# Kernel tuning notes

Measured on AMD Instinct MI355X. Metric: run time of the kernel, lower is better.

Reference implementation:

```python
import jax, jax.numpy as jnp
import numpy as np
from jax import lax

B, C, H, W = 2, 128, 192, 192
HEADS, WS, SS = 4, 8, 4
HID = 256  # int(C * expansion=2.0)
EPS = 1e-6


def _rpe_index(ws):
    coords = np.stack(np.meshgrid(np.arange(ws), np.arange(ws), indexing='ij')).reshape(2, -1)
    rel = (coords[:, :, None] - coords[:, None, :]).transpose(1, 2, 0)
    rel[:, :, 0] += ws - 1
    rel[:, :, 1] += ws - 1
    rel[:, :, 0] *= 2 * ws - 1
    return rel.sum(-1)  # (ws^2, ws^2) int index into rpe_table

RPE_IDX = _rpe_index(WS)


def _attn_mask(hp, wp, ws, ss):
    # Swin-style shifted-window mask, built once for static (hp, wp).
    img = np.zeros((hp, wp))
    cnt = 0
    for hs in (slice(0, -ws), slice(-ws, -ss), slice(-ss, None)):
        for wsl in (slice(0, -ws), slice(-ws, -ss), slice(-ss, None)):
            img[hs, wsl] = cnt
            cnt += 1
    mw = img.reshape(hp // ws, ws, wp // ws, ws).transpose(0, 2, 1, 3).reshape(-1, ws * ws)
    am = mw[:, None, :] - mw[:, :, None]
    return np.where(am != 0, -np.inf, 0.0).astype(np.float32)

MASK = jnp.asarray(_attn_mask(H, W, WS, SS))  # (nW, T, T)


def rmsnorm(x, s, b):
    # RMSNorm2d: variance over channel dim, computed in fp32.
    var = jnp.mean(jnp.square(x.astype(jnp.float32)), axis=1, keepdims=True)
    rms = jnp.sqrt(var + EPS).astype(x.dtype)
    return s[None, :, None, None] * x / rms + b[None, :, None, None]


def conv1x1(x, w, b):
    return jnp.einsum('oc,bchw->bohw', w, x) + b[None, :, None, None]


def dwconv3x3(x, w, b):
    y = lax.conv_general_dilated(x, w, (1, 1), 'SAME', feature_group_count=w.shape[0],
                                 dimension_numbers=('NCHW', 'OIHW', 'NCHW'))
    return y + b[None, :, None, None]


def gelu(x):
    return jax.nn.gelu(x, approximate=False)  # matches torch nn.GELU default (erf)


def conv_gated_block(x, s, b, w1, b1, wd, bd, w2, b2, beta):
    y = rmsnorm(x, s, b)
    y = conv1x1(y, w1, b1)
    y = dwconv3x3(y, wd, bd)
    u, v = jnp.split(y, 2, axis=1)
    y = conv1x1(u * gelu(v), w2, b2)
    return x + beta * y


def gated_ffn(x, s, b, w1, b1, w2, b2, gamma):
    y = rmsnorm(x, s, b)
    y = conv1x1(y, w1, b1)
    u, v = jnp.split(y, 2, axis=1)
    y = conv1x1(u * gelu(v), w2, b2)
    return x + gamma * y


def window_attention(x, qkv_w, qkv_b, rpe_table, proj_w, proj_b):
    b, c, h, w = x.shape
    hd = c // HEADS
    ws, ws2 = WS, WS * WS
    # H, W chosen divisible by ws, so _pad_to_window is a no-op here.
    x = jnp.roll(x, (-SS, -SS), axis=(2, 3))
    qkv = jnp.einsum('oc,bchw->bhwo', qkv_w, x) + qkv_b  # (B,H,W,3C)
    qkv = qkv.reshape(b, h // ws, ws, w // ws, ws, 3 * c).transpose(0, 1, 3, 2, 4, 5)
    qkv = qkv.reshape(-1, ws2, 3, HEADS, hd).transpose(2, 0, 3, 1, 4)  # (3, B*nW, nh, T, hd)
    q, k, v = qkv[0], qkv[1], qkv[2]
    attn = jnp.einsum('wnqd,wnkd->wnqk', q, k) * (hd ** -0.5)
    rpe = rpe_table[RPE_IDX.reshape(-1)].reshape(ws2, ws2, HEADS).transpose(2, 0, 1)  # (nh,T,T)
    nW = (h // ws) * (w // ws)
    attn = attn.reshape(b, nW, HEADS, ws2, ws2) + rpe[None, None] + MASK[None, :, None]
    attn = jax.nn.softmax(attn, axis=-1).reshape(-1, HEADS, ws2, ws2)
    out = jnp.einsum('wnqk,wnkd->wnqd', attn, v)
    out = out.transpose(0, 2, 1, 3).reshape(-1, ws2, c)
    out = out @ proj_w.T + proj_b  # nn.Linear
    out = out.reshape(b, h // ws, w // ws, ws, ws, c).transpose(0, 1, 3, 2, 4, 5).reshape(b, h, w, c)
    out = jnp.roll(out, (SS, SS), axis=(1, 2))
    return out.transpose(0, 3, 1, 2)


def setup_inputs():
    key = jax.random.key(0)
    ks = jax.random.split(key, 10)
    f = jnp.float32

    def nrm(k, shape, std=0.02):
        return jax.random.normal(k, shape, dtype=f) * std

    return {
        'x': jax.random.normal(ks[0], (B, C, H, W), dtype=f),
        'cg_s': jnp.ones((C,), f), 'cg_b': jnp.zeros((C,), f),
        'pw1_w': nrm(ks[1], (2 * HID, C)), 'pw1_b': jnp.zeros((2 * HID,), f),
        'dw_w': nrm(ks[2], (2 * HID, 1, 3, 3)), 'dw_b': jnp.zeros((2 * HID,), f),
        'pw2_w': nrm(ks[3], (C, HID)), 'pw2_b': jnp.zeros((C,), f),
        'beta': jnp.float32(0.5),
        'at_s': jnp.ones((C,), f), 'at_b': jnp.zeros((C,), f),
        'qkv_w': nrm(ks[4], (3 * C, C)), 'qkv_b': jnp.zeros((3 * C,), f),
        'rpe_table': nrm(ks[5], ((2 * WS - 1) ** 2, HEADS)),
        'proj_w': nrm(ks[6], (C, C)), 'proj_b': jnp.zeros((C,), f),
        'alpha': jnp.float32(0.5),
        'ff_s': jnp.ones((C,), f), 'ff_b': jnp.zeros((C,), f),
        'fc1_w': nrm(ks[7], (2 * HID, C)), 'fc1_b': jnp.zeros((2 * HID,), f),
        'fc2_w': nrm(ks[8], (C, HID)), 'fc2_b': jnp.zeros((C,), f),
        'gamma': jnp.float32(0.5),
    }


def reference(x, cg_s, cg_b, pw1_w, pw1_b, dw_w, dw_b, pw2_w, pw2_b, beta,
              at_s, at_b, qkv_w, qkv_b, rpe_table, proj_w, proj_b, alpha,
              ff_s, ff_b, fc1_w, fc1_b, fc2_w, fc2_b, gamma):
    x = conv_gated_block(x, cg_s, cg_b, pw1_w, pw1_b, dw_w, dw_b, pw2_w, pw2_b, beta)
    x = x + alpha * window_attention(rmsnorm(x, at_s, at_b), qkv_w, qkv_b, rpe_table, proj_w, proj_b)
    x = gated_ffn(x, ff_s, ff_b, fc1_w, fc1_b, fc2_w, fc2_b, gamma)
    return x
```

## Files before the change

kernel.cpp:

```cpp
#include <hip/hip_runtime.h>
#include <hip/hip_bf16.h>
#include <math.h>

#define HW   36864
#define BHW  73728

typedef float f32x4 __attribute__((ext_vector_type(4)));
typedef short short8 __attribute__((ext_vector_type(8)));
typedef short s16x4 __attribute__((ext_vector_type(4)));

__device__ __forceinline__ unsigned f2bf(float f) {
    unsigned u = __float_as_uint(f);
    return (u + 0x7fffu + ((u >> 16) & 1u)) >> 16;
}
__device__ __forceinline__ float bf2f(unsigned short s) {
    return __uint_as_float(((unsigned)s) << 16);
}
__device__ __forceinline__ float gelu_fast(float x) {
    float y = 1.5957691216057308f * fmaf(0.044715f * x * x, x, x);
    return x / (1.0f + __expf(-y));
}

__global__ __launch_bounds__(256)
void wconv_kernel(const float* __restrict__ w1, const float* __restrict__ w2,
                  const float* __restrict__ wq, const float* __restrict__ wp,
                  const float* __restrict__ wf1, const float* __restrict__ wf2,
                  const float* __restrict__ dww, const float* __restrict__ fb1,
                  ushort* __restrict__ o1, ushort* __restrict__ o2, ushort* __restrict__ oq,
                  ushort* __restrict__ op, ushort* __restrict__ of1, ushort* __restrict__ of2,
                  float* __restrict__ dwt, float* __restrict__ bg)
{
    int i = blockIdx.x * 256 + threadIdx.x;
    if      (i <  65536) o1 [i         ] = (ushort)f2bf(w1 [i         ]);
    else if (i <  98304) o2 [i -  65536] = (ushort)f2bf(w2 [i -  65536]);
    else if (i < 147456) oq [i -  98304] = (ushort)f2bf(wq [i -  98304]);
    else if (i < 163840) op [i - 147456] = (ushort)f2bf(wp [i - 147456]);
    else if (i < 229376) {
        int j = i - 163840;
        int col = j >> 7, k = j & 127;
        of1[j] = (ushort)f2bf(wf1[((size_t)((col & 1) * 256 + (col >> 1))) * 128 + k]);
    }
    else if (i < 262144) of2[i - 229376] = (ushort)f2bf(wf2[i - 229376]);
    else if (i < 266752) {
        int j = i - 262144;
        int tap = j >> 9, c = j & 511;
        dwt[j] = dww[c * 9 + tap];
    }
    else if (i < 267264) {
        int j = i - 266752;
        bg[j] = fb1[(j & 1) * 256 + (j >> 1)];
    }
}

__global__ __launch_bounds__(256)
void rmsnorm_t_kernel(const float* __restrict__ src, const float* __restrict__ s,
                      const float* __restrict__ bi, __hip_bfloat16* __restrict__ dst)
{
    int P = blockIdx.x * 256 + threadIdx.x;
    int b = P / HW, pp = P - b * HW;
    const float* xb = src + (size_t)b * 128 * HW + pp;
    float ss = 0.f;
#pragma unroll 8
    for (int c = 0; c < 128; ++c) { float v = xb[(size_t)c * HW]; ss = fmaf(v, v, ss); }
    float inv = 1.0f / sqrtf(ss * 0.0078125f + 1e-6f);
    unsigned* drow = (unsigned*)(dst + (size_t)P * 128);
#pragma unroll 4
    for (int c = 0; c < 128; c += 2) {
        float v0 = fmaf(s[c]     * xb[(size_t)c * HW],       inv, bi[c]);
        float v1 = fmaf(s[c + 1] * xb[(size_t)(c + 1) * HW], inv, bi[c + 1]);
        drow[c >> 1] = f2bf(v0) | (f2bf(v1) << 16);
    }
}

template<int K, int MODE>
__global__ __launch_bounds__(256)
void gemm_kernel(const __hip_bfloat16* __restrict__ Abf, const __hip_bfloat16* __restrict__ Wbf,
                 const float* __restrict__ bias, int N,
                 __hip_bfloat16* __restrict__ outb)
{
    __shared__ char smem[12288];
    short* sA = (short*)smem;
    short* sB = sA + 2048;

    const short* A = (const short*)Abf;
    const short* W = (const short*)Wbf;

    int t = threadIdx.x;
    int lane = t & 63, wv = t >> 6;
    int m0 = blockIdx.x * 64;
    int n0 = blockIdx.y * 128;
    int q = lane >> 4, r16 = lane & 15;

    f32x4 acc[4][2];
#pragma unroll
    for (int nt = 0; nt < 2; ++nt) {
        float bv = bias[n0 + wv * 32 + nt * 16 + r16];
#pragma unroll
        for (int mt = 0; mt < 4; ++mt) acc[mt][nt] = (f32x4){bv, bv, bv, bv};
    }

    for (int kk = 0; kk < K; kk += 32) {
        {
            int rbase = wv * 16;
            int row = rbase + (lane >> 2);
            int kc = (lane & 3) ^ ((row >> 1) & 3);
            const short* ga = A + (size_t)(m0 + row) * K + kk + kc * 8;
            __builtin_amdgcn_global_load_lds((const __attribute__((address_space(1))) void*)ga,
                                             (__attribute__((address_space(3))) void*)(sA + rbase * 32), 16, 0, 0);
        }
#pragma unroll
        for (int i = 0; i < 2; ++i) {
            int rbase = wv * 32 + i * 16;
            int row = rbase + (lane >> 2);
            int kc = (lane & 3) ^ ((row >> 1) & 3);
            const short* gb = W + (size_t)(n0 + row) * K + kk + kc * 8;
            __builtin_amdgcn_global_load_lds((const __attribute__((address_space(1))) void*)gb,
                                             (__attribute__((address_space(3))) void*)(sB + rbase * 32), 16, 0, 0);
        }
        __syncthreads();

        short8 af[4], bf[2];
#pragma unroll
        for (int mt = 0; mt < 4; ++mt) {
            int r = mt * 16 + r16;
            af[mt] = *(const short8*)(sA + (r * 4 + (q ^ ((r >> 1) & 3))) * 8);
        }
#pragma unroll
        for (int nt = 0; nt < 2; ++nt) {
            int r = wv * 32 + nt * 16 + r16;
            bf[nt] = *(const short8*)(sB + (r * 4 + (q ^ ((r >> 1) & 3))) * 8);
        }
#pragma unroll
        for (int mt = 0; mt < 4; ++mt)
#pragma unroll
            for (int nt = 0; nt < 2; ++nt)
                acc[mt][nt] = __builtin_amdgcn_mfma_f32_16x16x32_bf16(af[mt], bf[nt], acc[mt][nt], 0, 0, 0);
        __syncthreads();
    }

    if constexpr (MODE == 0) {
        ushort* ob = (ushort*)outb;
#pragma unroll
        for (int mt = 0; mt < 4; ++mt) {
            int row0 = m0 + mt * 16 + q * 4;
#pragma unroll
            for (int nt = 0; nt < 2; ++nt) {
                int col = n0 + wv * 32 + nt * 16 + r16;
#pragma unroll
                for (int rg = 0; rg < 4; ++rg)
                    ob[(size_t)(row0 + rg) * N + col] = (ushort)f2bf(acc[mt][nt][rg]);
            }
        }
    } else {
        ushort* ob = (ushort*)outb;
        int parity = r16 & 1;
#pragma unroll
        for (int mt = 0; mt < 4; ++mt) {
            int row0 = m0 + mt * 16 + q * 4;
#pragma unroll
            for (int nt = 0; nt < 2; ++nt) {
                int ch = (n0 + wv * 32 + nt * 16 + r16) >> 1;
#pragma unroll
                for (int rg = 0; rg < 4; ++rg) {
                    float val = acc[mt][nt][rg];
                    float part = __shfl_xor(val, 1);
                    float uu = parity ? part : val;
                    float vv = parity ? val : part;
                    float g = uu * gelu_fast(vv);
                    if (!parity)
                        ob[(size_t)(row0 + rg) * 256 + ch] = (ushort)f2bf(g);
                }
            }
        }
    }
}

template<int K, bool RMS>
__global__ __launch_bounds__(256)
void gemm_n128_kernel(const __hip_bfloat16* __restrict__ Abf, const __hip_bfloat16* __restrict__ Wbf,
                      const float* __restrict__ bias,
                      const float* __restrict__ rsrc, float* __restrict__ rdst,
                      const float* __restrict__ scale,
                      const float* __restrict__ rms_s, const float* __restrict__ rms_b,
                      __hip_bfloat16* __restrict__ xn)
{
    constexpr int SMEM = RMS ? 39424 : 34816;
    __shared__ char smem[SMEM];
    short* sA = (short*)smem;
    short* sB = sA + 2048;
    float* sEp = (float*)smem;
    float* sPar = (float*)(smem + 34816);
    float* sInv = (float*)(smem + 39168);

    const short* A = (const short*)Abf;
    const short* W = (const short*)Wbf;

    int t = threadIdx.x;
    int lane = t & 63, wv = t >> 6;
    int m0 = blockIdx.x * 64;
    int q = lane >> 4, r16 = lane & 15;

    f32x4 acc[4][2];
#pragma unroll
    for (int nt = 0; nt < 2; ++nt) {
        float bv = bias[wv * 32 + nt * 16 + r16];
#pragma unroll
        for (int mt = 0; mt < 4; ++mt) acc[mt][nt] = (f32x4){bv, bv, bv, bv};
    }

    for (int kk = 0; kk < K; kk += 32) {
        {
            int rbase = wv * 16;
            int row = rbase + (lane >> 2);
            int kc = (lane & 3) ^ ((row >> 1) & 3);
            const short* ga = A + (size_t)(m0 + row) * K + kk + kc * 8;
            __builtin_amdgcn_global_load_lds((const __attribute__((address_space(1))) void*)ga,
                                             (__attribute__((address_space(3))) void*)(sA + rbase * 32), 16, 0, 0);
        }
#pragma unroll
        for (int i = 0; i < 2; ++i) {
            int rbase = wv * 32 + i * 16;
            int row = rbase + (lane >> 2);
            int kc = (lane & 3) ^ ((row >> 1) & 3);
            const short* gb = W + (size_t)row * K + kk + kc * 8;
            __builtin_amdgcn_global_load_lds((const __attribute__((address_space(1))) void*)gb,
                                             (__attribute__((address_space(3))) void*)(sB + rbase * 32), 16, 0, 0);
        }
        __syncthreads();

        short8 af[4], bf[2];
#pragma unroll
        for (int mt = 0; mt < 4; ++mt) {
            int r = mt * 16 + r16;
            af[mt] = *(const short8*)(sA + (r * 4 + (q ^ ((r >> 1) & 3))) * 8);
        }
#pragma unroll
        for (int nt = 0; nt < 2; ++nt) {
            int r = wv * 32 + nt * 16 + r16;
            bf[nt] = *(const short8*)(sB + (r * 4 + (q ^ ((r >> 1) & 3))) * 8);
        }
#pragma unroll
        for (int mt = 0; mt < 4; ++mt)
#pragma unroll
            for (int nt = 0; nt < 2; ++nt)
                acc[mt][nt] = __builtin_amdgcn_mfma_f32_16x16x32_bf16(af[mt], bf[nt], acc[mt][nt], 0, 0, 0);
        __syncthreads();
    }

#pragma unroll
    for (int mt = 0; mt < 4; ++mt)
#pragma unroll
        for (int nt = 0; nt < 2; ++nt) {
            int c = wv * 32 + nt * 16 + r16;
            int px = mt * 16 + q * 4;
#pragma unroll
            for (int rg = 0; rg < 4; ++rg)
                sEp[c * 68 + px + rg] = acc[mt][nt][rg];
        }
    __syncthreads();

    int c16 = t >> 4, l16 = t & 15;
    int p0 = m0 + l16 * 4;
    int b = p0 / HW, pp = p0 - b * HW;
    float sc = scale[0];
    f32x4 ov[8];
    f32x4 ps = (f32x4){0.f, 0.f, 0.f, 0.f};
#pragma unroll
    for (int i = 0; i < 8; ++i) {
        int c = c16 + i * 16;
        f32x4 v = *(const f32x4*)&sEp[c * 68 + l16 * 4];
        size_t gi = (size_t)(b * 128 + c) * HW + pp;
        f32x4 r = *(const f32x4*)&rsrc[gi];
        f32x4 o = r + sc * v;
        *(f32x4*)&rdst[gi] = o;
        if constexpr (RMS) {
            ov[i] = o;
#pragma unroll
            for (int rg = 0; rg < 4; ++rg) ps[rg] = fmaf(o[rg], o[rg], ps[rg]);
        }
    }
    if constexpr (RMS) {
#pragma unroll
        for (int rg = 0; rg < 4; ++rg) sPar[(l16 * 4 + rg) * 17 + c16] = ps[rg];
        __syncthreads();
        if (t < 64) {
            float ssum = 0.f;
#pragma unroll
            for (int j = 0; j < 16; ++j) ssum += sPar[t * 17 + j];
            sInv[t] = 1.0f / sqrtf(ssum * 0.0078125f + 1e-6f);
        }
        __syncthreads();
        float iv[4];
#pragma unroll
        for (int rg = 0; rg < 4; ++rg) iv[rg] = sInv[l16 * 4 + rg];
        ushort* sXn = (ushort*)smem;
#pragma unroll
        for (int i = 0; i < 8; ++i) {
            int c = c16 + i * 16;
            float scs = rms_s[c], bcs = rms_b[c];
#pragma unroll
            for (int rg = 0; rg < 4; ++rg)
                sXn[(l16 * 4 + rg) * 132 + c] = (ushort)f2bf(fmaf(scs * ov[i][rg], iv[rg], bcs));
        }
        __syncthreads();
        {
            int px = t >> 2, qd = t & 3;
            const ushort* src = sXn + px * 132 + qd * 32;
            ushort* dst = (ushort*)xn + (size_t)(m0 + px) * 128 + qd * 32;
#pragma unroll
            for (int g = 0; g < 4; ++g)
                *(short8*)(dst + g * 8) = *(const short8*)(src + g * 8);
        }
    }
}

__global__ __launch_bounds__(256, 3)
void dwgate_kernel(const __hip_bfloat16* __restrict__ t1, const float* __restrict__ dwt,
                   const float* __restrict__ dwb, __hip_bfloat16* __restrict__ tg)
{
    int t = threadIdx.x;
    int tc = t & 63;
    int tp = t >> 6;
    int bx = blockIdx.x;
    int b = bx / 2304; int tt = bx % 2304;
    int th = tt / 48, tw = tt % 48;
    int h0 = th * 4, w = tw * 4 + tp;
    int cu = tc * 4;
    const ushort* t1u = (const ushort*)t1;

    f32x4 wu[9], wv[9];
#pragma unroll
    for (int tap = 0; tap < 9; ++tap) {
        wu[tap] = *(const f32x4*)(dwt + tap * 512 + cu);
        wv[tap] = *(const f32x4*)(dwt + tap * 512 + 256 + cu);
    }
    f32x4 bu = *(const f32x4*)(dwb + cu);
    f32x4 bv = *(const f32x4*)(dwb + 256 + cu);

    f32x4 au[4], av[4];
#pragma unroll
    for (int py = 0; py < 4; ++py) { au[py] = bu; av[py] = bv; }

#pragma unroll
    for (int r = 0; r < 6; ++r) {
        int hh = h0 - 1 + r;
        bool okr = (unsigned)hh < 192u;
        int hhc = okr ? hh : 0;
#pragma unroll
        for (int dxi = 0; dxi < 3; ++dxi) {
            int w2 = w + dxi - 1;
            bool ok = okr && ((unsigned)w2 < 192u);
            int w2c = (w2 < 0) ? 0 : ((w2 > 191) ? 191 : w2);
            const ushort* p = t1u + (size_t)(b * HW + hhc * 192 + w2c) * 512 + cu;
            s16x4 u4 = *(const s16x4*)p;
            s16x4 v4 = *(const s16x4*)(p + 256);
            f32x4 uf, vf;
#pragma unroll
            for (int e = 0; e < 4; ++e) {
                uf[e] = ok ? bf2f((ushort)u4[e]) : 0.f;
                vf[e] = ok ? bf2f((ushort)v4[e]) : 0.f;
            }
#pragma unroll
            for (int py = 0; py < 4; ++py) {
                int dy = r - 1 - py;
                if (dy < -1 || dy > 1) continue;
                int tap = (dy + 1) * 3 + dxi;
#pragma unroll
                for (int e = 0; e < 4; ++e) {
                    au[py][e] = fmaf(wu[tap][e], uf[e], au[py][e]);
                    av[py][e] = fmaf(wv[tap][e], vf[e], av[py][e]);
                }
            }
        }
    }
#pragma unroll
    for (int py = 0; py < 4; ++py) {
        s16x4 o4;
#pragma unroll
        for (int e = 0; e < 4; ++e) o4[e] = (short)(ushort)f2bf(au[py][e] * gelu_fast(av[py][e]));
        int gp = b * HW + (h0 + py) * 192 + w;
        *(s16x4*)((ushort*)tg + (size_t)gp * 256 + cu) = o4;
    }
}

__device__ __forceinline__ int wpix(int wh, int ww, int m) {
    int ty = m >> 3, tx = m & 7;
    int hs = wh * 8 + ty + 4; if (hs >= 192) hs -= 192;
    int wsc = ww * 8 + tx + 4; if (wsc >= 192) wsc -= 192;
    return hs * 192 + wsc;
}
__device__ __forceinline__ int wreg(int wh, int ww, int m) {
    int hr = wh * 8 + (m >> 3), wr = ww * 8 + (m & 7);
    return ((hr < 184) ? 0 : (hr < 188) ? 1 : 2) * 3 +
           ((wr < 184) ? 0 : (wr < 188) ? 1 : 2);
}

__global__ __launch_bounds__(256)
void attn_kernel(const __hip_bfloat16* __restrict__ qkv, const float* __restrict__ rpe,
                 __hip_bfloat16* __restrict__ attnout)
{
    __shared__ char smem[54288];
    int t = threadIdx.x;
    int lane = t & 63, head = t >> 6;
    int wh = blockIdx.x / 24, ww = blockIdx.x % 24;
    int b = blockIdx.y;
    int q = lane >> 4, r16 = lane & 15;

    float* rpe_s = (float*)(smem + 50688);
    for (int i = t; i < 900; i += 256) rpe_s[i] = rpe[i];

    char* Pbuf  = smem + head * 12672;
    char* VTbuf = Pbuf + 8448;
    const ushort* qkvu = (const ushort*)qkv;

    short8 aq[4], bk[4];
#pragma unroll
    for (int mt = 0; mt < 4; ++mt) {
        int pix = wpix(wh, ww, mt * 16 + r16);
        const ushort* rowp = qkvu + (size_t)(b * HW + pix) * 384 + head * 32 + q * 8;
        aq[mt] = *(const short8*)rowp;
        bk[mt] = *(const short8*)(rowp + 128);
    }
    {
        int pix = wpix(wh, ww, lane);
        const ushort* vp = qkvu + (size_t)(b * HW + pix) * 384 + 256 + head * 32;
        ushort* vt = (ushort*)VTbuf;
#pragma unroll
        for (int g = 0; g < 4; ++g) {
            short8 v8 = *(const short8*)(vp + g * 8);
#pragma unroll
            for (int e = 0; e < 8; ++e) vt[(g * 8 + e) * 66 + lane] = (ushort)v8[e];
        }
    }
    __syncthreads();

    f32x4 s[4][4];
#pragma unroll
    for (int mt = 0; mt < 4; ++mt)
#pragma unroll
        for (int nt = 0; nt < 4; ++nt) s[mt][nt] = (f32x4){0.f, 0.f, 0.f, 0.f};
#pragma unroll
    for (int mt = 0; mt < 4; ++mt)
#pragma unroll
        for (int nt = 0; nt < 4; ++nt)
            s[mt][nt] = __builtin_amdgcn_mfma_f32_16x16x32_bf16(aq[mt], bk[nt], s[mt][nt], 0, 0, 0);

    bool edge = (wh == 23) || (ww == 23);
    int tyj[4], txj[4], rgj[4];
#pragma unroll
    for (int nt = 0; nt < 4; ++nt) {
        int j = nt * 16 + r16;
        tyj[nt] = j >> 3; txj[nt] = j & 7;
        rgj[nt] = wreg(wh, ww, j);
    }
    float rinv[4][4];
#pragma unroll
    for (int mt = 0; mt < 4; ++mt) {
#pragma unroll
        for (int rg = 0; rg < 4; ++rg) {
            int i = mt * 16 + q * 4 + rg;
            int tyi = i >> 3, txi = i & 7;
            int rgi = edge ? wreg(wh, ww, i) : 0;
            float mx = -INFINITY;
#pragma unroll
            for (int nt = 0; nt < 4; ++nt) {
                float v = s[mt][nt][rg] * 0.17677669529663689f
                        + rpe_s[((tyi - tyj[nt] + 7) * 15 + (txi - txj[nt] + 7)) * 4 + head];
                if (edge && rgi != rgj[nt]) v = -INFINITY;
                s[mt][nt][rg] = v;
                mx = fmaxf(mx, v);
            }
            mx = fmaxf(mx, __shfl_xor(mx, 1));
            mx = fmaxf(mx, __shfl_xor(mx, 2));
            mx = fmaxf(mx, __shfl_xor(mx, 4));
            mx = fmaxf(mx, __shfl_xor(mx, 8));
            float sum = 0.f;
#pragma unroll
            for (int nt = 0; nt < 4; ++nt) {
                float e = __expf(s[mt][nt][rg] - mx);
                s[mt][nt][rg] = e;
                sum += e;
            }
            sum += __shfl_xor(sum, 1);
            sum += __shfl_xor(sum, 2);
            sum += __shfl_xor(sum, 4);
            sum += __shfl_xor(sum, 8);
            rinv[mt][rg] = 1.0f / sum;
        }
    }

    ushort* Pu = (ushort*)Pbuf;
#pragma unroll
    for (int mt = 0; mt < 4; ++mt)
#pragma unroll
        for (int rg = 0; rg < 4; ++rg) {
            int i = mt * 16 + q * 4 + rg;
#pragma unroll
            for (int nt = 0; nt < 4; ++nt)
                Pu[i * 66 + nt * 16 + r16] = (ushort)f2bf(s[mt][nt][rg]);
        }
    __syncthreads();

    f32x4 o[4][2];
#pragma unroll
    for (int mt = 0; mt < 4; ++mt) { o[mt][0] = (f32x4){0,0,0,0}; o[mt][1] = (f32x4){0,0,0,0}; }
    const uint* Pw = (const uint*)Pbuf;
    const uint* Vw = (const uint*)VTbuf;
#pragma unroll
    for (int ks = 0; ks < 2; ++ks) {
        short8 ap[4];
#pragma unroll
        for (int mt = 0; mt < 4; ++mt) {
            int base = (mt * 16 + r16) * 33 + ks * 16 + q * 4;
            uint d0 = Pw[base], d1 = Pw[base + 1], d2 = Pw[base + 2], d3 = Pw[base + 3];
            union { uint u[4]; short8 s8; } cv; cv.u[0] = d0; cv.u[1] = d1; cv.u[2] = d2; cv.u[3] = d3;
            ap[mt] = cv.s8;
        }
        short8 bv[2];
#pragma unroll
        for (int nt = 0; nt < 2; ++nt) {
            int base = (nt * 16 + r16) * 33 + ks * 16 + q * 4;
            uint d0 = Vw[base], d1 = Vw[base + 1], d2 = Vw[base + 2], d3 = Vw[base + 3];
            union { uint u[4]; short8 s8; } cv; cv.u[0] = d0; cv.u[1] = d1; cv.u[2] = d2; cv.u[3] = d3;
            bv[nt] = cv.s8;
        }
#pragma unroll
        for (int mt = 0; mt < 4; ++mt)
#pragma unroll
            for (int nt = 0; nt < 2; ++nt)
                o[mt][nt] = __builtin_amdgcn_mfma_f32_16x16x32_bf16(ap[mt], bv[nt], o[mt][nt], 0, 0, 0);
    }
    __syncthreads();

    float* Of = (float*)Pbuf;
#pragma unroll
    for (int mt = 0; mt < 4; ++mt)
#pragma unroll
        for (int rg = 0; rg < 4; ++rg) {
            int i = mt * 16 + q * 4 + rg;
            float sc = rinv[mt][rg];
            Of[i * 33 + r16]      = o[mt][0][rg] * sc;
            Of[i * 33 + 16 + r16] = o[mt][1][rg] * sc;
        }
    __syncthreads();
    {
        int pix = wpix(wh, ww, lane);
        ushort* ob = (ushort*)attnout + (size_t)(b * HW + pix) * 128 + head * 32;
#pragma unroll
        for (int g = 0; g < 4; ++g) {
            short8 o8;
#pragma unroll
            for (int e = 0; e < 8; ++e) o8[e] = (short)(ushort)f2bf(Of[lane * 33 + g * 8 + e]);
            *(short8*)(ob + g * 8) = o8;
        }
    }
}

extern "C" void kernel_launch(void* const* d_in, const int* in_sizes, int n_in,
                              void* d_out, int out_size, void* d_ws, size_t ws_size,
                              hipStream_t stream)
{
    const float* x     = (const float*)d_in[0];
    const float* cg_s  = (const float*)d_in[1];
    const float* cg_b  = (const float*)d_in[2];
    const float* pw1_w = (const float*)d_in[3];
    const float* pw1_b = (const float*)d_in[4];
    const float* dw_w  = (const float*)d_in[5];
    const float* dw_b  = (const float*)d_in[6];
    const float* pw2_w = (const float*)d_in[7];
    const float* pw2_b = (const float*)d_in[8];
    const float* beta  = (const float*)d_in[9];
    const float* at_s  = (const float*)d_in[10];
    const float* at_b  = (const float*)d_in[11];
    const float* qkv_w = (const float*)d_in[12];
    const float* qkv_b = (const float*)d_in[13];
    const float* rpe   = (const float*)d_in[14];
    const float* proj_w= (const float*)d_in[15];
    const float* proj_b= (const float*)d_in[16];
    const float* alpha = (const float*)d_in[17];
    const float* ff_s  = (const float*)d_in[18];
    const float* ff_b  = (const float*)d_in[19];
    const float* fc1_w = (const float*)d_in[20];
    const float* fc1_b = (const float*)d_in[21];
    const float* fc2_w = (const float*)d_in[22];
    const float* fc2_b = (const float*)d_in[23];
    const float* gamma = (const float*)d_in[24];
    float* out = (float*)d_out;

    char* ws = (char*)d_ws;
    __hip_bfloat16* Xn    = (__hip_bfloat16*)ws;
    __hip_bfloat16* t1    = (__hip_bfloat16*)(ws + 18874368);
    __hip_bfloat16* qkvb  = t1;
    __hip_bfloat16* tg    = (__hip_bfloat16*)(ws + 94371840);
    __hip_bfloat16* attno = tg;
    char* wsw = ws + 132120576;
    ushort* w1b  = (ushort*)(wsw);
    ushort* w2b  = (ushort*)(wsw + 131072);
    ushort* wqb  = (ushort*)(wsw + 196608);
    ushort* wpb  = (ushort*)(wsw + 294912);
    ushort* wf1b = (ushort*)(wsw + 327680);
    ushort* wf2b = (ushort*)(wsw + 458752);
    float*  dwt  = (float*) (wsw + 524288);
    float*  bg1  = (float*) (wsw + 542720);

    wconv_kernel<<<1044, 256, 0, stream>>>(pw1_w, pw2_w, qkv_w, proj_w, fc1_w, fc2_w, dw_w, fc1_b,
                                           w1b, w2b, wqb, wpb, wf1b, wf2b, dwt, bg1);

    rmsnorm_t_kernel<<<288, 256, 0, stream>>>(x, cg_s, cg_b, Xn);
    gemm_kernel<128, 0><<<dim3(1152, 4), 256, 0, stream>>>(Xn, (__hip_bfloat16*)w1b, pw1_b, 512, t1);
    dwgate_kernel<<<4608, 256, 0, stream>>>(t1, dwt, dw_b, tg);
    gemm_n128_kernel<256, true><<<1152, 256, 0, stream>>>(tg, (__hip_bfloat16*)w2b, pw2_b,
                                                          x, out, beta, at_s, at_b, Xn);

    gemm_kernel<128, 0><<<dim3(1152, 3), 256, 0, stream>>>(Xn, (__hip_bfloat16*)wqb, qkv_b, 384, qkvb);
    attn_kernel<<<dim3(576, 2), 256, 0, stream>>>(qkvb, rpe, attno);
    gemm_n128_kernel<128, true><<<1152, 256, 0, stream>>>(attno, (__hip_bfloat16*)wpb, proj_b,
                                                          out, out, alpha, ff_s, ff_b, Xn);

    gemm_kernel<128, 2><<<dim3(1152, 4), 256, 0, stream>>>(Xn, (__hip_bfloat16*)wf1b, bg1, 512, tg);
    gemm_n128_kernel<256, false><<<1152, 256, 0, stream>>>(tg, (__hip_bfloat16*)wf2b, fc2_b,
                                                           out, out, gamma, nullptr, nullptr, nullptr);
}
```

Measured before the change: 366.6 us.

## Preload full K tiles in GEMMs, split RMSNorm channels across waves, specialize dwconv edges

The GEMM kernels now stage the whole K extent of A and W in LDS with one barrier, or two 128-wide halves for K=256, instead of one barrier pair per 32-wide K step. They also add an occupancy hint of 3 blocks per CU. The RMSNorm transpose kernel spreads each pixel's 128 channels over four waves, keeps them in registers and reduces through shared memory, giving four times as many blocks. The depthwise-gate kernel gets a fast interior path with no bounds checks. The larger LDS footprint (up to 48 KB per block) may limit occupancy, and the GEMMs lose overlap between loads and MFMA within a block.

```diff
diff --git a/kernel.cpp b/kernel.cpp
--- a/kernel.cpp
+++ b/kernel.cpp
@@ -56,31 +56,48 @@
 void rmsnorm_t_kernel(const float* __restrict__ src, const float* __restrict__ s,
                       const float* __restrict__ bi, __hip_bfloat16* __restrict__ dst)
 {
-    int P = blockIdx.x * 256 + threadIdx.x;
+    __shared__ float sPar[4][64];
+    __shared__ float sInv[64];
+    int t = threadIdx.x, lane = t & 63, wv = t >> 6;
+    int P = blockIdx.x * 64 + lane;
     int b = P / HW, pp = P - b * HW;
     const float* xb = src + (size_t)b * 128 * HW + pp;
+    float v[32];
     float ss = 0.f;
-#pragma unroll 8
-    for (int c = 0; c < 128; ++c) { float v = xb[(size_t)c * HW]; ss = fmaf(v, v, ss); }
-    float inv = 1.0f / sqrtf(ss * 0.0078125f + 1e-6f);
-    unsigned* drow = (unsigned*)(dst + (size_t)P * 128);
-#pragma unroll 4
-    for (int c = 0; c < 128; c += 2) {
-        float v0 = fmaf(s[c]     * xb[(size_t)c * HW],       inv, bi[c]);
-        float v1 = fmaf(s[c + 1] * xb[(size_t)(c + 1) * HW], inv, bi[c + 1]);
-        drow[c >> 1] = f2bf(v0) | (f2bf(v1) << 16);
+#pragma unroll
+    for (int i = 0; i < 32; ++i) {
+        float x = xb[(size_t)(wv * 32 + i) * HW];
+        v[i] = x;
+        ss = fmaf(x, x, ss);
+    }
+    sPar[wv][lane] = ss;
+    __syncthreads();
+    if (t < 64) {
+        float tot = sPar[0][t] + sPar[1][t] + sPar[2][t] + sPar[3][t];
+        sInv[t] = 1.0f / sqrtf(tot * 0.0078125f + 1e-6f);
+    }
+    __syncthreads();
+    float inv = sInv[lane];
+    unsigned* drow = (unsigned*)(dst + (size_t)P * 128) + wv * 16;
+#pragma unroll
+    for (int i = 0; i < 32; i += 2) {
+        int c = wv * 32 + i;
+        float v0 = fmaf(s[c]     * v[i],     inv, bi[c]);
+        float v1 = fmaf(s[c + 1] * v[i + 1], inv, bi[c + 1]);
+        drow[i >> 1] = f2bf(v0) | (f2bf(v1) << 16);
     }
 }
 
 template<int K, int MODE>
-__global__ __launch_bounds__(256)
+__global__ __launch_bounds__(256, 3)
 void gemm_kernel(const __hip_bfloat16* __restrict__ Abf, const __hip_bfloat16* __restrict__ Wbf,
                  const float* __restrict__ bias, int N,
                  __hip_bfloat16* __restrict__ outb)
 {
-    __shared__ char smem[12288];
-    short* sA = (short*)smem;
-    short* sB = sA + 2048;
+    constexpr int STEPS = K / 32;
+    __shared__ __align__(16) short smem[(64 + 128) * K];
+    short* sA = smem;
+    short* sB = smem + 64 * K;
 
     const short* A = (const short*)Abf;
     const short* W = (const short*)Wbf;
@@ -99,43 +116,46 @@
         for (int mt = 0; mt < 4; ++mt) acc[mt][nt] = (f32x4){bv, bv, bv, bv};
     }
 
-    for (int kk = 0; kk < K; kk += 32) {
-        {
-            int rbase = wv * 16;
-            int row = rbase + (lane >> 2);
-            int kc = (lane & 3) ^ ((row >> 1) & 3);
-            const short* ga = A + (size_t)(m0 + row) * K + kk + kc * 8;
+    {
+        int lr = lane >> 2, lk = lane & 3;
+#pragma unroll
+        for (int st = 0; st < STEPS; ++st) {
+            int rowA = wv * 16 + lr;
+            int kcA = lk ^ ((rowA >> 1) & 3);
+            const short* ga = A + (size_t)(m0 + rowA) * K + st * 32 + kcA * 8;
             __builtin_amdgcn_global_load_lds((const __attribute__((address_space(1))) void*)ga,
-                                             (__attribute__((address_space(3))) void*)(sA + rbase * 32), 16, 0, 0);
-        }
-#pragma unroll
-        for (int i = 0; i < 2; ++i) {
-            int rbase = wv * 32 + i * 16;
-            int row = rbase + (lane >> 2);
-            int kc = (lane & 3) ^ ((row >> 1) & 3);
-            const short* gb = W + (size_t)(n0 + row) * K + kk + kc * 8;
-            __builtin_amdgcn_global_load_lds((const __attribute__((address_space(1))) void*)gb,
-                                             (__attribute__((address_space(3))) void*)(sB + rbase * 32), 16, 0, 0);
-        }
-        __syncthreads();
-
+                                             (__attribute__((address_space(3))) void*)(sA + st * 2048 + wv * 512), 16, 0, 0);
+#pragma unroll
+            for (int i = 0; i < 2; ++i) {
+                int rb = wv * 32 + i * 16;
+                int rowB = rb + lr;
+                int kcB = lk ^ ((rowB >> 1) & 3);
+                const short* gb = W + (size_t)(n0 + rowB) * K + st * 32 + kcB * 8;
+                __builtin_amdgcn_global_load_lds((const __attribute__((address_space(1))) void*)gb,
+                                                 (__attribute__((address_space(3))) void*)(sB + st * 4096 + rb * 32), 16, 0, 0);
+            }
+        }
+    }
+    __syncthreads();
+
+#pragma unroll
+    for (int st = 0; st < STEPS; ++st) {
         short8 af[4], bf[2];
 #pragma unroll
         for (int mt = 0; mt < 4; ++mt) {
             int r = mt * 16 + r16;
-            af[mt] = *(const short8*)(sA + (r * 4 + (q ^ ((r >> 1) & 3))) * 8);
+            af[mt] = *(const short8*)(sA + st * 2048 + (r * 4 + (q ^ ((r >> 1) & 3))) * 8);
         }
 #pragma unroll
         for (int nt = 0; nt < 2; ++nt) {
             int r = wv * 32 + nt * 16 + r16;
-            bf[nt] = *(const short8*)(sB + (r * 4 + (q ^ ((r >> 1) & 3))) * 8);
+            bf[nt] = *(const short8*)(sB + st * 4096 + (r * 4 + (q ^ ((r >> 1) & 3))) * 8);
         }
 #pragma unroll
         for (int mt = 0; mt < 4; ++mt)
 #pragma unroll
             for (int nt = 0; nt < 2; ++nt)
                 acc[mt][nt] = __builtin_amdgcn_mfma_f32_16x16x32_bf16(af[mt], bf[nt], acc[mt][nt], 0, 0, 0);
-        __syncthreads();
     }
 
     if constexpr (MODE == 0) {
@@ -176,7 +196,7 @@
 }
 
 template<int K, bool RMS>
-__global__ __launch_bounds__(256)
+__global__ __launch_bounds__(256, 3)
 void gemm_n128_kernel(const __hip_bfloat16* __restrict__ Abf, const __hip_bfloat16* __restrict__ Wbf,
                       const float* __restrict__ bias,
                       const float* __restrict__ rsrc, float* __restrict__ rdst,
@@ -184,10 +204,10 @@
                       const float* __restrict__ rms_s, const float* __restrict__ rms_b,
                       __hip_bfloat16* __restrict__ xn)
 {
-    constexpr int SMEM = RMS ? 39424 : 34816;
-    __shared__ char smem[SMEM];
+    constexpr int NH = K / 128;
+    __shared__ __align__(16) char smem[49152];
     short* sA = (short*)smem;
-    short* sB = sA + 2048;
+    short* sB = sA + 8192;
     float* sEp = (float*)smem;
     float* sPar = (float*)(smem + 34816);
     float* sInv = (float*)(smem + 39168);
@@ -208,44 +228,53 @@
         for (int mt = 0; mt < 4; ++mt) acc[mt][nt] = (f32x4){bv, bv, bv, bv};
     }
 
-    for (int kk = 0; kk < K; kk += 32) {
+#pragma unroll
+    for (int h = 0; h < NH; ++h) {
+        if (h) __syncthreads();
         {
-            int rbase = wv * 16;
-            int row = rbase + (lane >> 2);
-            int kc = (lane & 3) ^ ((row >> 1) & 3);
-            const short* ga = A + (size_t)(m0 + row) * K + kk + kc * 8;
-            __builtin_amdgcn_global_load_lds((const __attribute__((address_space(1))) void*)ga,
-                                             (__attribute__((address_space(3))) void*)(sA + rbase * 32), 16, 0, 0);
-        }
-#pragma unroll
-        for (int i = 0; i < 2; ++i) {
-            int rbase = wv * 32 + i * 16;
-            int row = rbase + (lane >> 2);
-            int kc = (lane & 3) ^ ((row >> 1) & 3);
-            const short* gb = W + (size_t)row * K + kk + kc * 8;
-            __builtin_amdgcn_global_load_lds((const __attribute__((address_space(1))) void*)gb,
-                                             (__attribute__((address_space(3))) void*)(sB + rbase * 32), 16, 0, 0);
+            int lr = lane >> 2, lk = lane & 3;
+#pragma unroll
+            for (int st = 0; st < 4; ++st) {
+                int kk = h * 128 + st * 32;
+                int rowA = wv * 16 + lr;
+                int kcA = lk ^ ((rowA >> 1) & 3);
+                const short* ga = A + (size_t)(m0 + rowA) * K + kk + kcA * 8;
+                __builtin_amdgcn_global_load_lds((const __attribute__((address_space(1))) void*)ga,
+                                                 (__attribute__((address_space(3))) void*)(sA + st * 2048 + wv * 512), 16, 0, 0);
+#pragma unroll
+                for (int i = 0; i < 2; ++i) {
+                    int rb = wv * 32 + i * 16;
+                    int rowB = rb + lr;
+                    int kcB = lk ^ ((rowB >> 1) & 3);
+                    const short* gb = W + (size_t)rowB * K + kk + kcB * 8;
+                    __builtin_amdgcn_global_load_lds((const __attribute__((address_space(1))) void*)gb,
+                                                     (__attribute__((address_space(3))) void*)(sB + st * 4096 + rb * 32), 16, 0, 0);
+                }
+            }
         }
         __syncthreads();
 
-        short8 af[4], bf[2];
-#pragma unroll
-        for (int mt = 0; mt < 4; ++mt) {
-            int r = mt * 16 + r16;
-            af[mt] = *(const short8*)(sA + (r * 4 + (q ^ ((r >> 1) & 3))) * 8);
-        }
-#pragma unroll
-        for (int nt = 0; nt < 2; ++nt) {
-            int r = wv * 32 + nt * 16 + r16;
-            bf[nt] = *(const short8*)(sB + (r * 4 + (q ^ ((r >> 1) & 3))) * 8);
-        }
-#pragma unroll
-        for (int mt = 0; mt < 4; ++mt)
-#pragma unroll
-            for (int nt = 0; nt < 2; ++nt)
-                acc[mt][nt] = __builtin_amdgcn_mfma_f32_16x16x32_bf16(af[mt], bf[nt], acc[mt][nt], 0, 0, 0);
-        __syncthreads();
-    }
+#pragma unroll
+        for (int st = 0; st < 4; ++st) {
+            short8 af[4], bf[2];
+#pragma unroll
+            for (int mt = 0; mt < 4; ++mt) {
+                int r = mt * 16 + r16;
+                af[mt] = *(const short8*)(sA + st * 2048 + (r * 4 + (q ^ ((r >> 1) & 3))) * 8);
+            }
+#pragma unroll
+            for (int nt = 0; nt < 2; ++nt) {
+                int r = wv * 32 + nt * 16 + r16;
+                bf[nt] = *(const short8*)(sB + st * 4096 + (r * 4 + (q ^ ((r >> 1) & 3))) * 8);
+            }
+#pragma unroll
+            for (int mt = 0; mt < 4; ++mt)
+#pragma unroll
+                for (int nt = 0; nt < 2; ++nt)
+                    acc[mt][nt] = __builtin_amdgcn_mfma_f32_16x16x32_bf16(af[mt], bf[nt], acc[mt][nt], 0, 0, 0);
+        }
+    }
+    __syncthreads();
 
 #pragma unroll
     for (int mt = 0; mt < 4; ++mt)
@@ -314,6 +343,48 @@
     }
 }
 
+template<bool EDGE>
+__device__ __forceinline__ void dw_body(const ushort* __restrict__ t1u,
+                                        int b, int h0, int w, int cu,
+                                        const f32x4* __restrict__ wu, const f32x4* __restrict__ wv,
+                                        f32x4* __restrict__ au, f32x4* __restrict__ av)
+{
+#pragma unroll
+    for (int r = 0; r < 6; ++r) {
+        int hh = h0 - 1 + r;
+        bool okr = EDGE ? ((unsigned)hh < 192u) : true;
+        int hhc = (EDGE && !okr) ? 0 : hh;
+#pragma unroll
+        for (int dxi = 0; dxi < 3; ++dxi) {
+            int w2 = w + dxi - 1;
+            bool ok = EDGE ? (okr && ((unsigned)w2 < 192u)) : true;
+            int w2c = EDGE ? ((w2 < 0) ? 0 : ((w2 > 191) ? 191 : w2)) : w2;
+            const ushort* p = t1u + (size_t)(b * HW + hhc * 192 + w2c) * 512 + cu;
+            s16x4 u4 = *(const s16x4*)p;
+            s16x4 v4 = *(const s16x4*)(p + 256);
+            f32x4 uf, vf;
+#pragma unroll
+            for (int e = 0; e < 4; ++e) {
+                float uu = bf2f((ushort)u4[e]);
+                float vv = bf2f((ushort)v4[e]);
+                uf[e] = (EDGE && !ok) ? 0.f : uu;
+                vf[e] = (EDGE && !ok) ? 0.f : vv;
+            }
+#pragma unroll
+            for (int py = 0; py < 4; ++py) {
+                int dy = r - 1 - py;
+                if (dy < -1 || dy > 1) continue;
+                int tap = (dy + 1) * 3 + dxi;
+#pragma unroll
+                for (int e = 0; e < 4; ++e) {
+                    au[py][e] = fmaf(wu[tap][e], uf[e], au[py][e]);
+                    av[py][e] = fmaf(wv[tap][e], vf[e], av[py][e]);
+                }
+            }
+        }
+    }
+}
+
 __global__ __launch_bounds__(256, 3)
 void dwgate_kernel(const __hip_bfloat16* __restrict__ t1, const float* __restrict__ dwt,
                    const float* __restrict__ dwb, __hip_bfloat16* __restrict__ tg)
@@ -341,38 +412,11 @@
 #pragma unroll
     for (int py = 0; py < 4; ++py) { au[py] = bu; av[py] = bv; }
 
-#pragma unroll
-    for (int r = 0; r < 6; ++r) {
-        int hh = h0 - 1 + r;
-        bool okr = (unsigned)hh < 192u;
-        int hhc = okr ? hh : 0;
-#pragma unroll
-        for (int dxi = 0; dxi < 3; ++dxi) {
-            int w2 = w + dxi - 1;
-            bool ok = okr && ((unsigned)w2 < 192u);
-            int w2c = (w2 < 0) ? 0 : ((w2 > 191) ? 191 : w2);
-            const ushort* p = t1u + (size_t)(b * HW + hhc * 192 + w2c) * 512 + cu;
-            s16x4 u4 = *(const s16x4*)p;
-            s16x4 v4 = *(const s16x4*)(p + 256);
-            f32x4 uf, vf;
-#pragma unroll
-            for (int e = 0; e < 4; ++e) {
-                uf[e] = ok ? bf2f((ushort)u4[e]) : 0.f;
-                vf[e] = ok ? bf2f((ushort)v4[e]) : 0.f;
-            }
-#pragma unroll
-            for (int py = 0; py < 4; ++py) {
-                int dy = r - 1 - py;
-                if (dy < -1 || dy > 1) continue;
-                int tap = (dy + 1) * 3 + dxi;
-#pragma unroll
-                for (int e = 0; e < 4; ++e) {
-                    au[py][e] = fmaf(wu[tap][e], uf[e], au[py][e]);
-                    av[py][e] = fmaf(wv[tap][e], vf[e], av[py][e]);
-                }
-            }
-        }
-    }
+    if (th > 0 && th < 47 && tw > 0 && tw < 47)
+        dw_body<false>(t1u, b, h0, w, cu, wu, wv, au, av);
+    else
+        dw_body<true >(t1u, b, h0, w, cu, wu, wv, au, av);
+
 #pragma unroll
     for (int py = 0; py < 4; ++py) {
         s16x4 o4;
@@ -606,7 +650,7 @@
     wconv_kernel<<<1044, 256, 0, stream>>>(pw1_w, pw2_w, qkv_w, proj_w, fc1_w, fc2_w, dw_w, fc1_b,
                                            w1b, w2b, wqb, wpb, wf1b, wf2b, dwt, bg1);
 
-    rmsnorm_t_kernel<<<288, 256, 0, stream>>>(x, cg_s, cg_b, Xn);
+    rmsnorm_t_kernel<<<1152, 256, 0, stream>>>(x, cg_s, cg_b, Xn);
     gemm_kernel<128, 0><<<dim3(1152, 4), 256, 0, stream>>>(Xn, (__hip_bfloat16*)w1b, pw1_b, 512, t1);
     dwgate_kernel<<<4608, 256, 0, stream>>>(t1, dwt, dw_b, tg);
     gemm_n128_kernel<256, true><<<1152, 256, 0, stream>>>(tg, (__hip_bfloat16*)w2b, pw2_b,
```

Measured after the change: 360.1 us. About the same (-1.8%).
